# Kernel tuning notes

Measured on AMD Instinct MI355X. Metric: run time of the kernel, lower is better.

## Reference

```python
import jax, jax.numpy as jnp
import numpy as np


def setup_inputs() -> dict:
    key = jax.random.key(0)
    ks = jax.random.split(key, 16)
    B, D, H = 65536, 64, 512
    s = 0.05
    inp = {
        "state": jax.random.normal(ks[0], (B, D), dtype=jnp.float32),
        "Wz0": jax.random.normal(ks[1], (H, D), dtype=jnp.float32) * s,
        "bz0": jax.random.normal(ks[2], (H,), dtype=jnp.float32) * s,
        "Wz1": jax.random.normal(ks[3], (H, H), dtype=jnp.float32) * s,
        "Wz2": jax.random.normal(ks[4], (H, H), dtype=jnp.float32) * s,
        "Wz3": jax.random.normal(ks[5], (H, H), dtype=jnp.float32) * s,
        "WzL": jax.random.normal(ks[6], (1, H), dtype=jnp.float32) * s,
        "Wx0": jax.random.normal(ks[7], (H, D), dtype=jnp.float32) * s,
        "bx0": jax.random.normal(ks[8], (H,), dtype=jnp.float32) * s,
        "Wx1": jax.random.normal(ks[9], (H, D), dtype=jnp.float32) * s,
        "bx1": jax.random.normal(ks[10], (H,), dtype=jnp.float32) * s,
        "Wx2": jax.random.normal(ks[11], (H, D), dtype=jnp.float32) * s,
        "bx2": jax.random.normal(ks[12], (H,), dtype=jnp.float32) * s,
        "WxL": jax.random.normal(ks[13], (1, D), dtype=jnp.float32) * s,
    }
    return inp


def reference(state, Wz0, bz0, Wz1, Wz2, Wz3, WzL, Wx0, bx0, Wx1, bx1, Wx2, bx2, WxL):
    sp = jax.nn.softplus

    def icnn_sum(x):  # x: [B, D] -> scalar (sum of per-sample convex outputs)
        z = sp(x @ Wz0.T + bz0)                      # [B, H]
        z = sp(z @ Wz1.T + x @ Wx0.T + bx0)          # [B, H]
        z = sp(z @ Wz2.T + x @ Wx1.T + bx1)          # [B, H]
        z = sp(z @ Wz3.T + x @ Wx2.T + bx2)          # [B, H]
        out = z @ WzL.T + x @ WxL.T                  # [B, 1]
        return out.sum()

    x = state - 1.0
    # Output is scalar per-sample, so grad of the batch-sum equals the stacked
    # per-sample jacobians computed by the torch Python loop.
    action = jax.grad(icnn_sum)(x)                   # [B, D]
    return action
```

## Files before the change

kernel.cpp:

```cpp
#include <hip/hip_runtime.h>

typedef unsigned short u16;
typedef unsigned int u32;
typedef unsigned long long u64;

#define B_TOTAL 65536
#define H 512
#define D 64
#define BM 64

typedef __bf16 bf16x8 __attribute__((ext_vector_type(8)));
typedef float f32x4 __attribute__((ext_vector_type(4)));

__device__ __forceinline__ u32 f2b(float f) {
  u32 u = __builtin_bit_cast(u32, f);
  return (u + 0x7fffu + ((u >> 16) & 1u)) >> 16;
}
__device__ __forceinline__ float b2f(u32 bits) {
  return __builtin_bit_cast(float, bits << 16);
}

#define OFF_Wz0b 0
#define OFF_Wx0b 32768
#define OFF_Wx1b 65536
#define OFF_Wx2b 98304
#define OFF_Wz1b 131072
#define OFF_Wz2b 393216
#define OFF_Wz3b 655360
#define OFF_Wz1t 917504
#define OFF_Wz2t 1179648
#define OFF_Wz3t 1441792
#define OFF_Wz0t 1703936
#define OFF_Wx0t 1736704
#define OFF_Wx1t 1769472
#define OFF_Wx2t 1802240
#define OFF_WEND 1835008
#define SLAB_ELEMS (B_TOTAL * H)
#define OFF_S0 OFF_WEND
#define OFF_S1 (OFF_S0 + SLAB_ELEMS)
#define OFF_S2 (OFF_S1 + SLAB_ELEMS)
#define WS_ELEMS (OFF_S2 + SLAB_ELEMS)

__global__ __launch_bounds__(256) void prep_kernel(
    const float* __restrict__ Wz0, const float* __restrict__ Wz1,
    const float* __restrict__ Wz2, const float* __restrict__ Wz3,
    const float* __restrict__ Wx0, const float* __restrict__ Wx1,
    const float* __restrict__ Wx2, u16* __restrict__ wsb) {
  int i = blockIdx.x * 256 + threadIdx.x;
  const float* src;
  int NN, KK, trans, p;
  if (i < 131072) {
    int r = i >> 15; p = i & 32767;
    src = (r == 0) ? Wz0 : (r == 1) ? Wx0 : (r == 2) ? Wx1 : Wx2;
    NN = 512; KK = 64; trans = 0;
  } else if (i < 917504) {
    int j = i - 131072; int r = j >> 18; p = j & 262143;
    src = (r == 0) ? Wz1 : (r == 1) ? Wz2 : Wz3;
    NN = 512; KK = 512; trans = 0;
  } else if (i < 1703936) {
    int j = i - 917504; int r = j >> 18; p = j & 262143;
    src = (r == 0) ? Wz1 : (r == 1) ? Wz2 : Wz3;
    NN = 512; KK = 512; trans = 1;
  } else {
    int j = i - 1703936; int r = j >> 15; p = j & 32767;
    src = (r == 0) ? Wz0 : (r == 1) ? Wx0 : (r == 2) ? Wx1 : Wx2;
    NN = 64; KK = 512; trans = 1;
  }
  int jj = p & 7, lane = (p >> 3) & 63, blk = p >> 9;
  int kt_sh = (KK == 64) ? 1 : 4;
  int ntile = blk >> kt_sh;
  int kstep = blk & ((1 << kt_sh) - 1);
  int n = ntile * 16 + (lane & 15);
  int k = kstep * 32 + ((lane >> 4) << 3) + jj;
  float v = trans ? src[k * NN + n] : src[n * KK + k];
  wsb[i] = (u16)f2b(v);
}

__global__ __launch_bounds__(256) void fill_sentinel(float* out, int n) {
  int i = blockIdx.x * 256 + threadIdx.x;
  if (i < n) out[i] = 12345.0f;
}

__global__ __launch_bounds__(1024, 4) void icnn_kernel(
    const float* __restrict__ state,
    const float* __restrict__ bz0, const float* __restrict__ bx0,
    const float* __restrict__ bx1, const float* __restrict__ bx2,
    const float* __restrict__ WzL, const float* __restrict__ WxL,
    u16* __restrict__ wsw, float* __restrict__ out) {
  __shared__ u16 zbuf[BM * H];
  __shared__ u16 wbuf[2 * 16384];
  __shared__ u16 xbuf[BM * 72];

  const int tid = threadIdx.x;
  const int w = tid >> 6;
  const int lane = tid & 63;
  const int l15 = lane & 15;
  const int q = lane >> 4;
  const int blk = blockIdx.x;

  const u16* Wz0b = wsw + OFF_Wz0b;
  const u16* Wx0b = wsw + OFF_Wx0b;
  const u16* Wx1b = wsw + OFF_Wx1b;
  const u16* Wx2b = wsw + OFF_Wx2b;
  const u16* Wz1b = wsw + OFF_Wz1b;
  const u16* Wz2b = wsw + OFF_Wz2b;
  const u16* Wz3b = wsw + OFF_Wz3b;
  const u16* Wz1t = wsw + OFF_Wz1t;
  const u16* Wz2t = wsw + OFF_Wz2t;
  const u16* Wz3t = wsw + OFF_Wz3t;
  const u16* Wz0t = wsw + OFF_Wz0t;
  const u16* Wx0t = wsw + OFF_Wx0t;
  const u16* Wx1t = wsw + OFF_Wx1t;
  const u16* Wx2t = wsw + OFF_Wx2t;
  u64* slab0 = (u64*)(wsw + OFF_S0);
  u64* slab1 = (u64*)(wsw + OFF_S1);
  u64* slab2 = (u64*)(wsw + OFF_S2);

  auto lbar = [&]() {
    asm volatile("s_waitcnt lgkmcnt(0)" ::: "memory");
    __builtin_amdgcn_s_barrier();
    asm volatile("" ::: "memory");
  };

  {
    int r = tid >> 4, c0 = (tid & 15) << 2;
    const float* p = state + (blk * BM + r) * D + c0;
    f32x4 v = __builtin_nontemporal_load((const f32x4*)p);
    u32* dst = (u32*)&xbuf[r * 72 + c0];
    dst[0] = f2b(v[0] - 1.0f) | (f2b(v[1] - 1.0f) << 16);
    dst[1] = f2b(v[2] - 1.0f) | (f2b(v[3] - 1.0f) << 16);
  }

  f32x4 acc[4][2];
  const f32x4 Z = {0.f, 0.f, 0.f, 0.f};
  f32x4 pk = Z;

  auto ldA = [&](int mt, int step) -> bf16x8 {
    return *(const bf16x8*)(&zbuf[(step * 4 + mt) * 512 + q * 128 + l15 * 8]);
  };
  auto ldX = [&](int mt, int ks) -> bf16x8 {
    return *(const bf16x8*)(&xbuf[(mt * 16 + l15) * 72 + ks * 32 + q * 8]);
  };
  auto wrZ = [&](int row, int n, u16 bits) {
    zbuf[((n >> 5) * 4 + (row >> 4)) * 512 + ((n >> 3) & 3) * 128 +
         (row & 15) * 8 + (n & 7)] = bits;
  };

  auto stageW = [&](const u16* Wp, int st, int buf) {
    const u16* gb = Wp + ((w * 2) * 16 + st) * 512 + lane * 8;
    u16* lb = &wbuf[buf * 16384 + (w * 2) * 512];
#pragma unroll
    for (int j = 0; j < 2; ++j)
      __builtin_amdgcn_global_load_lds(
          (const __attribute__((address_space(1))) void*)(gb + j * 16 * 512),
          (__attribute__((address_space(3))) void*)(lb + j * 512), 16, 0, 0);
  };

  auto fwdX = [&](const u16* Wxp, bool zero_first) {
    const u16* xb = Wxp + lane * 8;
#pragma unroll
    for (int ks = 0; ks < 2; ++ks) {
      bf16x8 b2[2];
#pragma unroll
      for (int nt = 0; nt < 2; ++nt)
        b2[nt] = *(const bf16x8*)(xb + ((w * 2 + nt) * 2 + ks) * 512);
#pragma unroll
      for (int mt = 0; mt < 4; ++mt) {
        bf16x8 ax = ldX(mt, ks);
#pragma unroll
        for (int nt = 0; nt < 2; ++nt) {
          f32x4 c = (zero_first && ks == 0) ? Z : acc[mt][nt];
          acc[mt][nt] = __builtin_amdgcn_mfma_f32_16x16x32_bf16(ax, b2[nt], c, 0, 0, 0);
        }
      }
    }
  };

  auto fwdH = [&](const u16* Wp) {
#pragma unroll
    for (int st = 0; st < 16; ++st) {
      if (st < 15) {
        stageW(Wp, st + 1, (st + 1) & 1);
        asm volatile("s_waitcnt vmcnt(2)" ::: "memory");
      } else {
        asm volatile("s_waitcnt vmcnt(0)" ::: "memory");
      }
      const u16* wb = &wbuf[(st & 1) * 16384 + (w * 2) * 512 + lane * 8];
      bf16x8 a[4];
#pragma unroll
      for (int mt = 0; mt < 4; ++mt) a[mt] = ldA(mt, st);
#pragma unroll
      for (int nt = 0; nt < 2; ++nt) {
        bf16x8 b = *(const bf16x8*)(wb + nt * 512);
#pragma unroll
        for (int mt = 0; mt < 4; ++mt)
          acc[mt][nt] = __builtin_amdgcn_mfma_f32_16x16x32_bf16(
              a[mt], b, (st == 0) ? Z : acc[mt][nt], 0, 0, 0);
      }
    }
  };

  auto fwd_epi = [&](const float* biasp, u64* slab) {
    float bias[2];
#pragma unroll
    for (int nt = 0; nt < 2; ++nt) bias[nt] = biasp[(w * 2 + nt) * 16 + l15];
#pragma unroll
    for (int mt = 0; mt < 4; ++mt)
#pragma unroll
      for (int nt = 0; nt < 2; ++nt) {
        int n = (w * 2 + nt) * 16 + l15;
        f32x4 A = acc[mt][nt];
        u64 pack = 0;
#pragma unroll
        for (int r = 0; r < 4; ++r) {
          float a = A[r] + bias[nt];
          float t = __expf(-a);
          float u = 1.0f + t;
          float s = __builtin_amdgcn_rcpf(u);
          float z = a + __logf(u);
          pack |= (u64)f2b(s) << (16 * r);
          wrZ(mt * 16 + q * 4 + r, n, (u16)f2b(z));
        }
        slab[((blk * 16 + w) * 8 + mt * 2 + nt) * 64 + lane] = pack;
      }
  };
  auto d3_epi = [&](const float* biasp) {
    float bias[2], wl[2];
#pragma unroll
    for (int nt = 0; nt < 2; ++nt) {
      bias[nt] = biasp[(w * 2 + nt) * 16 + l15];
      wl[nt] = WzL[(w * 2 + nt) * 16 + l15];
    }
#pragma unroll
    for (int mt = 0; mt < 4; ++mt)
#pragma unroll
      for (int nt = 0; nt < 2; ++nt) {
        int n = (w * 2 + nt) * 16 + l15;
        f32x4 A = acc[mt][nt];
#pragma unroll
        for (int r = 0; r < 4; ++r) {
          float a = A[r] + bias[nt];
          float t = __expf(-a);
          float s = __builtin_amdgcn_rcpf(1.0f + t);
          wrZ(mt * 16 + q * 4 + r, n, (u16)f2b(wl[nt] * s));
        }
      }
  };
  auto bwd_epi = [&](const u64* slab) {
    u64 v[4][2];
#pragma unroll
    for (int mt = 0; mt < 4; ++mt)
#pragma unroll
      for (int nt = 0; nt < 2; ++nt)
        v[mt][nt] = slab[((blk * 16 + w) * 8 + mt * 2 + nt) * 64 + lane];
#pragma unroll
    for (int mt = 0; mt < 4; ++mt)
#pragma unroll
      for (int nt = 0; nt < 2; ++nt) {
        int n = (w * 2 + nt) * 16 + l15;
        f32x4 A = acc[mt][nt];
#pragma unroll
        for (int r = 0; r < 4; ++r) {
          float s = b2f((u32)(v[mt][nt] >> (16 * r)) & 0xffffu);
          wrZ(mt * 16 + q * 4 + r, n, (u16)f2b(A[r] * s));
        }
      }
  };

  auto minigrad = [&](const u16* Wg, bool init) {
    int rt = w & 3, ct = w >> 2;
    const u16* gb = Wg + lane * 8;
    f32x4 t = init ? Z : pk;
#pragma unroll 4
    for (int st = 0; st < 16; ++st) {
      bf16x8 a = ldA(rt, st);
      bf16x8 g = *(const bf16x8*)(gb + (ct * 16 + st) * 512);
      t = __builtin_amdgcn_mfma_f32_16x16x32_bf16(a, g, t, 0, 0, 0);
    }
    pk = t;
  };

  lbar();
  fwdX(Wz0b, true);
  stageW(Wz1b, 0, 0);
  fwd_epi(bz0, slab0);
  lbar();
  fwdH(Wz1b); fwdX(Wx0b, false);
  lbar();
  stageW(Wz2b, 0, 0);
  fwd_epi(bx0, slab1);
  lbar();
  fwdH(Wz2b); fwdX(Wx1b, false);
  lbar();
  stageW(Wz3b, 0, 0);
  fwd_epi(bx1, slab2);
  lbar();
  fwdH(Wz3b); fwdX(Wx2b, false);
  lbar();
  stageW(Wz3t, 0, 0);
  d3_epi(bx2);
  lbar();
  minigrad(Wx2t, true);
  fwdH(Wz3t);
  lbar();
  stageW(Wz2t, 0, 0);
  bwd_epi(slab2);
  lbar();
  minigrad(Wx1t, false);
  fwdH(Wz2t);
  lbar();
  stageW(Wz1t, 0, 0);
  bwd_epi(slab1);
  lbar();
  minigrad(Wx0t, false);
  fwdH(Wz1t);
  lbar();
  bwd_epi(slab0);
  lbar();
  minigrad(Wz0t, false);
  {
    int rt = w & 3, ct = w >> 2;
    float wx = WxL[ct * 16 + l15];
#pragma unroll
    for (int r = 0; r < 4; ++r) {
      int row = blk * BM + rt * 16 + q * 4 + r;
      out[row * D + ct * 16 + l15] = pk[r] + wx;
    }
  }
}

extern "C" void kernel_launch(void* const* d_in, const int* in_sizes, int n_in,
                              void* d_out, int out_size, void* d_ws, size_t ws_size,
                              hipStream_t stream) {
  const float* state = (const float*)d_in[0];
  const float* Wz0 = (const float*)d_in[1];
  const float* bz0 = (const float*)d_in[2];
  const float* Wz1 = (const float*)d_in[3];
  const float* Wz2 = (const float*)d_in[4];
  const float* Wz3 = (const float*)d_in[5];
  const float* WzL = (const float*)d_in[6];
  const float* Wx0 = (const float*)d_in[7];
  const float* bx0 = (const float*)d_in[8];
  const float* Wx1 = (const float*)d_in[9];
  const float* bx1 = (const float*)d_in[10];
  const float* Wx2 = (const float*)d_in[11];
  const float* bx2 = (const float*)d_in[12];
  const float* WxL = (const float*)d_in[13];

  if (ws_size < (size_t)WS_ELEMS * 2) {
    fill_sentinel<<<(out_size + 255) / 256, 256, 0, stream>>>((float*)d_out, out_size);
    return;
  }
  u16* wsw = (u16*)d_ws;
  prep_kernel<<<OFF_WEND / 256, 256, 0, stream>>>(Wz0, Wz1, Wz2, Wz3, Wx0, Wx1, Wx2, wsw);
  icnn_kernel<<<B_TOTAL / BM, 1024, 0, stream>>>(state, bz0, bx0, bx1, bx2, WzL, WxL,
                                                 wsw, (float*)d_out);
}
```

Before: 494.2 us.

## Ping-pong activation buffers in LDS and load weights directly into registers

The kernel drops the LDS weight staging buffer that was filled with global_load_lds. Weight fragments are now read straight from global memory (L2-resident) into registers, prefetching one k-step ahead, and the inner loop is no longer unrolled. The freed LDS becomes a second activation buffer, so each layer reads one buffer and writes its epilogue into the other. This removes half the per-layer barriers and the staging sync, at the cost of per-wave global load latency and lower weight reuse across waves.

```diff
diff --git a/kernel.cpp b/kernel.cpp
--- a/kernel.cpp
+++ b/kernel.cpp
@@ -87,8 +87,8 @@
     const float* __restrict__ bx1, const float* __restrict__ bx2,
     const float* __restrict__ WzL, const float* __restrict__ WxL,
     u16* __restrict__ wsw, float* __restrict__ out) {
-  __shared__ u16 zbuf[BM * H];
-  __shared__ u16 wbuf[2 * 16384];
+  __shared__ u16 zbA[BM * H];
+  __shared__ u16 zbB[BM * H];
   __shared__ u16 xbuf[BM * 72];
 
   const int tid = threadIdx.x;
@@ -135,28 +135,18 @@
   const f32x4 Z = {0.f, 0.f, 0.f, 0.f};
   f32x4 pk = Z;
 
-  auto ldA = [&](int mt, int step) -> bf16x8 {
-    return *(const bf16x8*)(&zbuf[(step * 4 + mt) * 512 + q * 128 + l15 * 8]);
+  auto ldA = [&](const u16* zb, int mt, int step) -> bf16x8 {
+    return *(const bf16x8*)(&zb[(step * 4 + mt) * 512 + q * 128 + l15 * 8]);
   };
   auto ldX = [&](int mt, int ks) -> bf16x8 {
     return *(const bf16x8*)(&xbuf[(mt * 16 + l15) * 72 + ks * 32 + q * 8]);
   };
-  auto wrZ = [&](int row, int n, u16 bits) {
-    zbuf[((n >> 5) * 4 + (row >> 4)) * 512 + ((n >> 3) & 3) * 128 +
-         (row & 15) * 8 + (n & 7)] = bits;
-  };
-
-  auto stageW = [&](const u16* Wp, int st, int buf) {
-    const u16* gb = Wp + ((w * 2) * 16 + st) * 512 + lane * 8;
-    u16* lb = &wbuf[buf * 16384 + (w * 2) * 512];
-#pragma unroll
-    for (int j = 0; j < 2; ++j)
-      __builtin_amdgcn_global_load_lds(
-          (const __attribute__((address_space(1))) void*)(gb + j * 16 * 512),
-          (__attribute__((address_space(3))) void*)(lb + j * 512), 16, 0, 0);
-  };
-
-  auto fwdX = [&](const u16* Wxp, bool zero_first) {
+  auto wrZ = [&](u16* zb, int row, int n, u16 bits) {
+    zb[((n >> 5) * 4 + (row >> 4)) * 512 + ((n >> 3) & 3) * 128 +
+       (row & 15) * 8 + (n & 7)] = bits;
+  };
+
+  auto fwdX = [&](const u16* Wxp) {
     const u16* xb = Wxp + lane * 8;
 #pragma unroll
     for (int ks = 0; ks < 2; ++ks) {
@@ -169,38 +159,38 @@
         bf16x8 ax = ldX(mt, ks);
 #pragma unroll
         for (int nt = 0; nt < 2; ++nt) {
-          f32x4 c = (zero_first && ks == 0) ? Z : acc[mt][nt];
+          f32x4 c = (ks == 0) ? Z : acc[mt][nt];
           acc[mt][nt] = __builtin_amdgcn_mfma_f32_16x16x32_bf16(ax, b2[nt], c, 0, 0, 0);
         }
       }
     }
   };
 
-  auto fwdH = [&](const u16* Wp) {
-#pragma unroll
+  auto fwdH = [&](const u16* Wp, const u16* zb, bool zero) {
+    const u16* gb = Wp + (w * 2 * 16) * 512 + lane * 8;
+    bf16x8 bc0 = *(const bf16x8*)(gb);
+    bf16x8 bc1 = *(const bf16x8*)(gb + 16 * 512);
+#pragma unroll 1
     for (int st = 0; st < 16; ++st) {
-      if (st < 15) {
-        stageW(Wp, st + 1, (st + 1) & 1);
-        asm volatile("s_waitcnt vmcnt(2)" ::: "memory");
-      } else {
-        asm volatile("s_waitcnt vmcnt(0)" ::: "memory");
-      }
-      const u16* wb = &wbuf[(st & 1) * 16384 + (w * 2) * 512 + lane * 8];
+      int stn = (st < 15) ? st + 1 : st;
+      bf16x8 bn0 = *(const bf16x8*)(gb + stn * 512);
+      bf16x8 bn1 = *(const bf16x8*)(gb + (16 + stn) * 512);
       bf16x8 a[4];
 #pragma unroll
-      for (int mt = 0; mt < 4; ++mt) a[mt] = ldA(mt, st);
-#pragma unroll
-      for (int nt = 0; nt < 2; ++nt) {
-        bf16x8 b = *(const bf16x8*)(wb + nt * 512);
-#pragma unroll
-        for (int mt = 0; mt < 4; ++mt)
-          acc[mt][nt] = __builtin_amdgcn_mfma_f32_16x16x32_bf16(
-              a[mt], b, (st == 0) ? Z : acc[mt][nt], 0, 0, 0);
-      }
-    }
-  };
-
-  auto fwd_epi = [&](const float* biasp, u64* slab) {
+      for (int mt = 0; mt < 4; ++mt) a[mt] = ldA(zb, mt, st);
+#pragma unroll
+      for (int mt = 0; mt < 4; ++mt)
+        acc[mt][0] = __builtin_amdgcn_mfma_f32_16x16x32_bf16(
+            a[mt], bc0, (zero && st == 0) ? Z : acc[mt][0], 0, 0, 0);
+#pragma unroll
+      for (int mt = 0; mt < 4; ++mt)
+        acc[mt][1] = __builtin_amdgcn_mfma_f32_16x16x32_bf16(
+            a[mt], bc1, (zero && st == 0) ? Z : acc[mt][1], 0, 0, 0);
+      bc0 = bn0; bc1 = bn1;
+    }
+  };
+
+  auto fwd_epi = [&](const float* biasp, u64* slab, u16* zb) {
     float bias[2];
 #pragma unroll
     for (int nt = 0; nt < 2; ++nt) bias[nt] = biasp[(w * 2 + nt) * 16 + l15];
@@ -219,12 +209,12 @@
           float s = __builtin_amdgcn_rcpf(u);
           float z = a + __logf(u);
           pack |= (u64)f2b(s) << (16 * r);
-          wrZ(mt * 16 + q * 4 + r, n, (u16)f2b(z));
+          wrZ(zb, mt * 16 + q * 4 + r, n, (u16)f2b(z));
         }
         slab[((blk * 16 + w) * 8 + mt * 2 + nt) * 64 + lane] = pack;
       }
   };
-  auto d3_epi = [&](const float* biasp) {
+  auto d3_epi = [&](const float* biasp, u16* zb) {
     float bias[2], wl[2];
 #pragma unroll
     for (int nt = 0; nt < 2; ++nt) {
@@ -242,11 +232,11 @@
           float a = A[r] + bias[nt];
           float t = __expf(-a);
           float s = __builtin_amdgcn_rcpf(1.0f + t);
-          wrZ(mt * 16 + q * 4 + r, n, (u16)f2b(wl[nt] * s));
+          wrZ(zb, mt * 16 + q * 4 + r, n, (u16)f2b(wl[nt] * s));
         }
       }
   };
-  auto bwd_epi = [&](const u64* slab) {
+  auto bwd_epi = [&](const u64* slab, u16* zb) {
     u64 v[4][2];
 #pragma unroll
     for (int mt = 0; mt < 4; ++mt)
@@ -262,18 +252,18 @@
 #pragma unroll
         for (int r = 0; r < 4; ++r) {
           float s = b2f((u32)(v[mt][nt] >> (16 * r)) & 0xffffu);
-          wrZ(mt * 16 + q * 4 + r, n, (u16)f2b(A[r] * s));
+          wrZ(zb, mt * 16 + q * 4 + r, n, (u16)f2b(A[r] * s));
         }
       }
   };
 
-  auto minigrad = [&](const u16* Wg, bool init) {
+  auto minigrad = [&](const u16* Wg, const u16* zb, bool init) {
     int rt = w & 3, ct = w >> 2;
     const u16* gb = Wg + lane * 8;
     f32x4 t = init ? Z : pk;
 #pragma unroll 4
     for (int st = 0; st < 16; ++st) {
-      bf16x8 a = ldA(rt, st);
+      bf16x8 a = ldA(zb, rt, st);
       bf16x8 g = *(const bf16x8*)(gb + (ct * 16 + st) * 512);
       t = __builtin_amdgcn_mfma_f32_16x16x32_bf16(a, g, t, 0, 0, 0);
     }
@@ -281,43 +271,31 @@
   };
 
   lbar();
-  fwdX(Wz0b, true);
-  stageW(Wz1b, 0, 0);
-  fwd_epi(bz0, slab0);
-  lbar();
-  fwdH(Wz1b); fwdX(Wx0b, false);
-  lbar();
-  stageW(Wz2b, 0, 0);
-  fwd_epi(bx0, slab1);
-  lbar();
-  fwdH(Wz2b); fwdX(Wx1b, false);
-  lbar();
-  stageW(Wz3b, 0, 0);
-  fwd_epi(bx1, slab2);
-  lbar();
-  fwdH(Wz3b); fwdX(Wx2b, false);
-  lbar();
-  stageW(Wz3t, 0, 0);
-  d3_epi(bx2);
-  lbar();
-  minigrad(Wx2t, true);
-  fwdH(Wz3t);
-  lbar();
-  stageW(Wz2t, 0, 0);
-  bwd_epi(slab2);
-  lbar();
-  minigrad(Wx1t, false);
-  fwdH(Wz2t);
-  lbar();
-  stageW(Wz1t, 0, 0);
-  bwd_epi(slab1);
-  lbar();
-  minigrad(Wx0t, false);
-  fwdH(Wz1t);
-  lbar();
-  bwd_epi(slab0);
-  lbar();
-  minigrad(Wz0t, false);
+  fwdX(Wz0b);
+  fwd_epi(bz0, slab0, zbA);
+  lbar();
+  fwdX(Wx0b); fwdH(Wz1b, zbA, false);
+  fwd_epi(bx0, slab1, zbB);
+  lbar();
+  fwdX(Wx1b); fwdH(Wz2b, zbB, false);
+  fwd_epi(bx1, slab2, zbA);
+  lbar();
+  fwdX(Wx2b); fwdH(Wz3b, zbA, false);
+  d3_epi(bx2, zbB);
+  lbar();
+  minigrad(Wx2t, zbB, true);
+  fwdH(Wz3t, zbB, true);
+  bwd_epi(slab2, zbA);
+  lbar();
+  minigrad(Wx1t, zbA, false);
+  fwdH(Wz2t, zbA, true);
+  bwd_epi(slab1, zbB);
+  lbar();
+  minigrad(Wx0t, zbB, false);
+  fwdH(Wz1t, zbB, true);
+  bwd_epi(slab0, zbA);
+  lbar();
+  minigrad(Wz0t, zbA, false);
   {
     int rt = w & 3, ct = w >> 2;
     float wx = WxL[ct * 16 + l15];
```

New measurement: 441.8 us. 10.6% less time.
